# Kernel optimization log

Hardware: AMD Instinct MI355X
Metric: run time of the kernel (lower is better)

Reference implementation:

```python
import jax, jax.numpy as jnp
import numpy as np

VOCAB, EMB, HID, NTAG, SEQ = 50000, 256, 512, 20, 8192
H = HID // 2  # per-direction hidden size


def _lstm_dir(x, Wih, Whh, bih, bhh, reverse):
    # x: [S, E]; PyTorch gate order i, f, g, o
    h0 = jnp.zeros((H,), x.dtype)
    c0 = jnp.zeros((H,), x.dtype)
    b = bih + bhh
    xg = x @ Wih.T + b  # [S, 4H] precompute input projection

    def step(carry, xt):
        h, c = carry
        gates = xt + h @ Whh.T
        i, f, g, o = jnp.split(gates, 4)
        i = jax.nn.sigmoid(i)
        f = jax.nn.sigmoid(f)
        g = jnp.tanh(g)
        o = jax.nn.sigmoid(o)
        c = f * c + i * g
        h = o * jnp.tanh(c)
        return (h, c), h

    _, hs = jax.lax.scan(step, (h0, c0), xg, reverse=reverse)
    return hs  # [S, H]


def _viterbi(emissions, start_trans, end_trans, trans):
    # emissions [S, T]; torchcrf-style Viterbi decode
    score0 = start_trans + emissions[0]

    def fwd(score, em):
        tot = score[:, None] + trans          # [T_from, T_to]
        bp = jnp.argmax(tot, axis=0)          # best previous tag per next tag
        score = jnp.max(tot, axis=0) + em
        return score, bp

    final, bps = jax.lax.scan(fwd, score0, emissions[1:])
    final = final + end_trans
    last = jnp.argmax(final).astype(jnp.int32)

    def back(tag, bp):
        prev = bp[tag].astype(jnp.int32)
        return prev, prev

    _, prevs = jax.lax.scan(back, last, bps, reverse=True)
    return jnp.concatenate([prevs, last[None]])  # [S]


def setup_inputs() -> dict:
    key = jax.random.key(0)
    ks = jax.random.split(key, 16)
    s = 0.1
    inp = {
        "sentence": jax.random.randint(ks[0], (SEQ,), 0, VOCAB, dtype=jnp.int64)
                    if jax.config.read("jax_enable_x64") else
                    jax.random.randint(ks[0], (SEQ,), 0, VOCAB, dtype=jnp.int32),
        "embed": jax.random.normal(ks[1], (VOCAB, EMB), jnp.float32),
        "Wih_f": jax.random.normal(ks[2], (4 * H, EMB), jnp.float32) * s,
        "Whh_f": jax.random.normal(ks[3], (4 * H, H), jnp.float32) * s,
        "bih_f": jax.random.normal(ks[4], (4 * H,), jnp.float32) * s,
        "bhh_f": jax.random.normal(ks[5], (4 * H,), jnp.float32) * s,
        "Wih_b": jax.random.normal(ks[6], (4 * H, EMB), jnp.float32) * s,
        "Whh_b": jax.random.normal(ks[7], (4 * H, H), jnp.float32) * s,
        "bih_b": jax.random.normal(ks[8], (4 * H,), jnp.float32) * s,
        "bhh_b": jax.random.normal(ks[9], (4 * H,), jnp.float32) * s,
        "Wout": jax.random.normal(ks[10], (NTAG, HID), jnp.float32) * s,
        "bout": jax.random.normal(ks[11], (NTAG,), jnp.float32) * s,
        "start_trans": jax.random.normal(ks[12], (NTAG,), jnp.float32) * s,
        "end_trans": jax.random.normal(ks[13], (NTAG,), jnp.float32) * s,
        "trans": jax.random.normal(ks[14], (NTAG, NTAG), jnp.float32) * s,
    }
    return inp


def reference(sentence, embed, Wih_f, Whh_f, bih_f, bhh_f,
              Wih_b, Whh_b, bih_b, bhh_b, Wout, bout,
              start_trans, end_trans, trans):
    x = embed[sentence]                                  # [S, E]
    h_f = _lstm_dir(x, Wih_f, Whh_f, bih_f, bhh_f, reverse=False)
    h_b = _lstm_dir(x, Wih_b, Whh_b, bih_b, bhh_b, reverse=True)
    lstm_out = jnp.concatenate([h_f, h_b], axis=-1)      # [S, HID]; dropout is eval-mode identity
    emissions = lstm_out @ Wout.T + bout                 # [S, T]
    path = _viterbi(emissions, start_trans, end_trans, trans)
    return path
```

## Files before the change

### kernel.cpp

```cpp
#include <hip/hip_runtime.h>
#include <hip/hip_bf16.h>


#define S    8192
#define E    256
#define Hh   256
#define G    1024
#define NT   20
#define NB   4
#define NCHUNK 128
#define CLEN   64
#define SENT 0x7FC0DEADu

__global__ __launch_bounds__(256) void sentinel_fill(unsigned int* __restrict__ lo_u)
{
    size_t base = (size_t)blockIdx.x * 1024 + threadIdx.x;
    #pragma unroll
    for (int i = 0; i < 4; ++i)
        __hip_atomic_store(&lo_u[base + (size_t)i * 256], SENT,
                           __ATOMIC_RELAXED, __HIP_MEMORY_SCOPE_AGENT);
}

__global__ __launch_bounds__(1024, 4) void xg_project(
    const int* __restrict__ sent, const float* __restrict__ embed,
    const float* __restrict__ Wih_f, const float* __restrict__ bih_f, const float* __restrict__ bhh_f,
    const float* __restrict__ Wih_b, const float* __restrict__ bih_b, const float* __restrict__ bhh_b,
    float* __restrict__ xg)
{
    const int tb  = blockIdx.x;
    const int rb  = blockIdx.y;
    const int dir = blockIdx.z;
    const int tid = threadIdx.x;
    const int q   = tid >> 8;
    const int idx = tid & 255;
    const int r   = rb * 256 + idx;
    const float* Wih = dir ? Wih_b : Wih_f;

    __shared__ __align__(16) float4 xs4[32 * 64];
    __shared__ float psum[1024];

    const int t0 = tb * 32;
    #pragma unroll
    for (int i = 0; i < 2; ++i) {
        int qq  = i * 1024 + tid;
        int row = qq >> 6;
        int c4  = qq & 63;
        int widx = sent[t0 + row];
        xs4[qq] = *(const float4*)(embed + (size_t)widx * E + (size_t)c4 * 4);
    }

    float w[64];
    #pragma unroll
    for (int k = 0; k < 64; k += 4) {
        float4 v = *(const float4*)(Wih + (size_t)r * E + q * 64 + k);
        w[k] = v.x; w[k+1] = v.y; w[k+2] = v.z; w[k+3] = v.w;
    }
    float bias = 0.f;
    if (tid < 256) bias = dir ? (bih_b[r] + bhh_b[r]) : (bih_f[r] + bhh_f[r]);
    __syncthreads();

    const float* xs = (const float*)xs4 + q * 64;
    float* outb = xg + ((size_t)dir * S + t0) * G + r;
    for (int tt = 0; tt < 32; ++tt) {
        float a0 = 0.f, a1 = 0.f, a2 = 0.f, a3 = 0.f;
        #pragma unroll
        for (int k = 0; k < 64; k += 4) {
            float4 h4 = *(const float4*)(xs + tt * E + k);
            a0 = fmaf(w[k],   h4.x, a0);
            a1 = fmaf(w[k+1], h4.y, a1);
            a2 = fmaf(w[k+2], h4.z, a2);
            a3 = fmaf(w[k+3], h4.w, a3);
        }
        psum[tid] = (a0 + a1) + (a2 + a3);
        __syncthreads();
        if (tid < 256)
            outb[(size_t)tt * G] = bias +
                ((psum[idx] + psum[idx + 256]) + (psum[idx + 512] + psum[idx + 768]));
        __syncthreads();
    }
}

__global__ __launch_bounds__(1024, 4) void lstm_scan_mc(
    const float* __restrict__ xg,
    const float* __restrict__ Whh_f,
    const float* __restrict__ Whh_b,
    float* __restrict__ out)
{
    const int b    = blockIdx.x;
    const int dir  = blockIdx.y;
    const int tid  = threadIdx.x;
    const int q    = tid >> 8;
    const int idx  = tid & 255;
    const int gate = idx >> 6;
    const int hloc = idx & 63;
    const int hidx = b * 64 + hloc;
    const int row  = gate * Hh + hidx;
    const float* W   = dir ? Whh_b : Whh_f;
    const float* xgd = xg + (size_t)dir * S * G;

    float w[64];
    #pragma unroll
    for (int k = 0; k < 64; k += 4) {
        float4 v = *(const float4*)(W + (size_t)row * Hh + q * 64 + k);
        w[k] = v.x; w[k+1] = v.y; w[k+2] = v.z; w[k+3] = v.w;
    }

    __shared__ __align__(16) float h_lds[Hh];
    __shared__ float psum[1024];
    __shared__ float gates_lds[256];
    if (tid < Hh) h_lds[tid] = 0.f;
    float c = 0.f;

    const int t0 = dir ? (S - 1) : 0;
    const int dt = dir ? -1 : 1;
    float xg_cur = (tid < 256) ? xgd[(size_t)t0 * G + row] : 0.f;
    __syncthreads();

    for (int s = 0; s < S; ++s) {
        const int t = t0 + dt * s;
        float xg_next = 0.f;
        if (tid < 256 && s + 1 < S) xg_next = xgd[(size_t)(t + dt) * G + row];

        const float* hh = (const float*)h_lds + q * 64;
        float a0 = 0.f, a1 = 0.f, a2 = 0.f, a3 = 0.f;
        #pragma unroll
        for (int k = 0; k < 64; k += 4) {
            float4 h4 = *(const float4*)(hh + k);
            a0 = fmaf(w[k],   h4.x, a0);
            a1 = fmaf(w[k+1], h4.y, a1);
            a2 = fmaf(w[k+2], h4.z, a2);
            a3 = fmaf(w[k+3], h4.w, a3);
        }
        psum[tid] = (a0 + a1) + (a2 + a3);
        __syncthreads();

        if (tid < 256) {
            float acc = xg_cur +
                ((psum[idx] + psum[idx + 256]) + (psum[idx + 512] + psum[idx + 768]));
            float a = (gate == 2) ? tanhf(acc) : 1.f / (1.f + expf(-acc));
            gates_lds[idx] = a;
        }
        __syncthreads();

        if (tid < 64) {
            float iv = gates_lds[hloc];
            float fv = gates_lds[64 + hloc];
            float gv = gates_lds[128 + hloc];
            float ov = gates_lds[192 + hloc];
            c = fv * c + iv * gv;
            float h = ov * tanhf(c);
            __hip_atomic_store(out + (size_t)t * 512 + dir * Hh + hidx, h,
                               __ATOMIC_RELAXED, __HIP_MEMORY_SCOPE_AGENT);
            h_lds[hidx] = h;
        }
        if (s + 1 < S && tid < Hh && (tid >> 6) != b) {
            const unsigned int* srcp =
                (const unsigned int*)(out + (size_t)t * 512 + dir * Hh + tid);
            unsigned int v;
            do {
                v = __hip_atomic_load(srcp, __ATOMIC_RELAXED,
                                      __HIP_MEMORY_SCOPE_AGENT);
            } while (v == SENT);
            h_lds[tid] = __uint_as_float(v);
        }
        __syncthreads();
        xg_cur = xg_next;
    }
}

__global__ __launch_bounds__(256) void emissions_kernel(
    const float* __restrict__ lo,
    const float* __restrict__ Wout,
    const float* __restrict__ bout,
    float* __restrict__ em)
{
    int gid = blockIdx.x * blockDim.x + threadIdx.x;
    if (gid >= S * NT) return;
    int t = gid / NT;
    int j = gid - t * NT;
    const float* x = lo + (size_t)t * 512;
    const float* w = Wout + (size_t)j * 512;
    float a0 = 0.f, a1 = 0.f, a2 = 0.f, a3 = 0.f;
    #pragma unroll 8
    for (int k = 0; k < 512; k += 4) {
        float4 xv = *(const float4*)(x + k);
        float4 wv = *(const float4*)(w + k);
        a0 = fmaf(xv.x, wv.x, a0);
        a1 = fmaf(xv.y, wv.y, a1);
        a2 = fmaf(xv.z, wv.z, a2);
        a3 = fmaf(xv.w, wv.w, a3);
    }
    em[gid] = bout[j] + ((a0 + a1) + (a2 + a3));
}

__global__ __launch_bounds__(64) void viterbi_fwd(
    const float* __restrict__ em,
    const float* __restrict__ start_trans,
    const float* __restrict__ end_trans,
    const float* __restrict__ trans,
    unsigned char* __restrict__ bp,
    int* __restrict__ last_out)
{
    const int lane = threadIdx.x;
    const int g    = lane / 20;
    const int j    = lane - g * 20;
    const int i0   = g * 7;

    float tc[7];
    #pragma unroll
    for (int u = 0; u < 7; ++u) {
        int i = i0 + u;
        tc[u] = (g < 3 && i < 20) ? trans[i * NT + j] : -3.0e38f;
    }

    const int jj = (g < 3) ? j : 0;
    float snew  = start_trans[jj] + em[jj];
    if (g == 0) bp[j] = (unsigned char)j;
    float e_cur = em[NT + jj];

    for (int t = 1; t < S; ++t) {
        float s_sub[7];
        #pragma unroll
        for (int u = 0; u < 7; ++u)
            s_sub[u] = __shfl(snew, i0 + u);
        float e_nxt = (t + 1 < S) ? em[(size_t)(t + 1) * NT + jj] : 0.f;

        float bv = s_sub[0] + tc[0];
        int   bi = i0;
        #pragma unroll
        for (int u = 1; u < 7; ++u) {
            float v = s_sub[u] + tc[u];
            if (v > bv) { bv = v; bi = i0 + u; }
        }
        float v0 = __shfl(bv, jj), v1 = __shfl(bv, jj + 20), v2 = __shfl(bv, jj + 40);
        int   c0 = __shfl(bi, jj), c1 = __shfl(bi, jj + 20), c2 = __shfl(bi, jj + 40);
        float best = v0; int bidx = c0;
        if (v1 > best) { best = v1; bidx = c1; }
        if (v2 > best) { best = v2; bidx = c2; }
        snew = best + e_cur;
        if (g == 0) bp[(size_t)t * NT + j] = (unsigned char)bidx;
        e_cur = e_nxt;
    }

    float bv = __shfl(snew, 0) + end_trans[0];
    int   bi = 0;
    #pragma unroll 1
    for (int i = 1; i < 20; ++i) {
        float v = __shfl(snew, i) + end_trans[i];
        if (v > bv) { bv = v; bi = i; }
    }
    if (lane == 0) *last_out = bi;
}

__global__ __launch_bounds__(64) void bt_maps(
    const unsigned char* __restrict__ bp, unsigned char* __restrict__ maps)
{
    __shared__ unsigned char lbp[CLEN * NT];
    const int c = blockIdx.x, tid = threadIdx.x;
    const unsigned* src = (const unsigned*)(bp + (size_t)c * CLEN * NT);
    unsigned* dst = (unsigned*)lbp;
    for (int q = tid; q < CLEN * NT / 4; q += 64) dst[q] = src[q];
    __syncthreads();
    if (tid < NT) {
        int x = tid;
        for (int t = CLEN - 1; t >= 0; --t) x = lbp[t * NT + x];
        maps[c * NT + tid] = (unsigned char)x;
    }
}

__global__ __launch_bounds__(64) void bt_boundary(
    const unsigned char* __restrict__ maps, const int* __restrict__ last_out,
    int* __restrict__ btags)
{
    __shared__ unsigned char m[NCHUNK * NT];
    const int tid = threadIdx.x;
    for (int q = tid; q < NCHUNK * NT; q += 64) m[q] = maps[q];
    __syncthreads();
    if (tid == 0) {
        int x = *last_out;
        btags[NCHUNK - 1] = x;
        for (int c = NCHUNK - 1; c >= 1; --c) {
            x = m[c * NT + x];
            btags[c - 1] = x;
        }
    }
}

__global__ __launch_bounds__(64) void bt_emit(
    const unsigned char* __restrict__ bp, const int* __restrict__ btags,
    int* __restrict__ path)
{
    __shared__ unsigned char lbp[CLEN * NT];
    const int c = blockIdx.x, tid = threadIdx.x;
    const unsigned* src = (const unsigned*)(bp + (size_t)c * CLEN * NT);
    unsigned* dst = (unsigned*)lbp;
    for (int q = tid; q < CLEN * NT / 4; q += 64) dst[q] = src[q];
    __syncthreads();
    if (tid == 0) {
        int x = btags[c];
        path[c * CLEN + CLEN - 1] = x;
        for (int t = CLEN - 1; t >= 1; --t) {
            x = lbp[t * NT + x];
            path[c * CLEN + t - 1] = x;
        }
    }
}

extern "C" void kernel_launch(void* const* d_in, const int* in_sizes, int n_in,
                              void* d_out, int out_size, void* d_ws, size_t ws_size,
                              hipStream_t stream) {
    const int*   sent   = (const int*)  d_in[0];
    const float* embed  = (const float*)d_in[1];
    const float* Wih_f  = (const float*)d_in[2];
    const float* Whh_f  = (const float*)d_in[3];
    const float* bih_f  = (const float*)d_in[4];
    const float* bhh_f  = (const float*)d_in[5];
    const float* Wih_b  = (const float*)d_in[6];
    const float* Whh_b  = (const float*)d_in[7];
    const float* bih_b  = (const float*)d_in[8];
    const float* bhh_b  = (const float*)d_in[9];
    const float* Wout   = (const float*)d_in[10];
    const float* bout   = (const float*)d_in[11];
    const float* start_trans = (const float*)d_in[12];
    const float* end_trans   = (const float*)d_in[13];
    const float* trans       = (const float*)d_in[14];
    int* path = (int*)d_out;

    char* ws = (char*)d_ws;
    size_t off = 0;
    float* xg = (float*)(ws + off); off += (size_t)2 * S * G * 4;
    float* lo = (float*)(ws + off); off += (size_t)S * 512 * 4;
    float* em = (float*)(ws + off); off += (size_t)S * NT * 4;
    unsigned char* bp   = (unsigned char*)(ws + off); off += (size_t)S * NT;
    unsigned char* maps = (unsigned char*)(ws + off); off += 4096;
    int* btags = (int*)(ws + off); off += 1024;
    int* lastp = (int*)(ws + off); off += 256;

    sentinel_fill<<<dim3(4096), 256, 0, stream>>>((unsigned int*)lo);
    xg_project<<<dim3(S / 32, 4, 2), 1024, 0, stream>>>(
        sent, embed, Wih_f, bih_f, bhh_f, Wih_b, bih_b, bhh_b, xg);
    lstm_scan_mc<<<dim3(NB, 2), 1024, 0, stream>>>(xg, Whh_f, Whh_b, lo);
    emissions_kernel<<<dim3((S * NT + 255) / 256), 256, 0, stream>>>(lo, Wout, bout, em);
    viterbi_fwd<<<dim3(1), 64, 0, stream>>>(em, start_trans, end_trans, trans, bp, lastp);
    bt_maps<<<dim3(NCHUNK), 64, 0, stream>>>(bp, maps);
    bt_boundary<<<dim3(1), 64, 0, stream>>>(maps, lastp, btags);
    bt_emit<<<dim3(NCHUNK), 64, 0, stream>>>(bp, btags, path);
}
```

Measured before the change: 15.61 ms.

## Co-locate LSTM scan workgroups on one XCC and use cheaper cross-block polling

```diff
diff --git a/kernel.cpp b/kernel.cpp
--- a/kernel.cpp
+++ b/kernel.cpp
@@ -8,17 +8,42 @@
 #define G    1024
 #define NT   20
 #define NB   4
+#define NCAND 64
 #define NCHUNK 128
 #define CLEN   64
 #define SENT 0x7FC0DEADu
 
+struct ScanCtl {
+    int cnt[16];
+    int winner;
+};
+
+__device__ __forceinline__ int get_xcc_id() {
+    int x;
+    asm volatile("s_getreg_b32 %0, hwreg(HW_REG_XCC_ID)" : "=s"(x));
+    return x & 0xf;
+}
+
+__device__ __forceinline__ unsigned ld_sc0_u32(const void* p) {
+    unsigned v;
+    asm volatile("global_load_dword %0, %1, off sc0\n"
+                 "s_waitcnt vmcnt(0)"
+                 : "=v"(v) : "v"(p) : "memory");
+    return v;
+}
+
+__global__ __launch_bounds__(64) void init_ctl(ScanCtl* __restrict__ ctl)
+{
+    if (threadIdx.x < 16) ctl->cnt[threadIdx.x] = 0;
+    if (threadIdx.x == 0) ctl->winner = -1;
+}
+
 __global__ __launch_bounds__(256) void sentinel_fill(unsigned int* __restrict__ lo_u)
 {
     size_t base = (size_t)blockIdx.x * 1024 + threadIdx.x;
     #pragma unroll
     for (int i = 0; i < 4; ++i)
-        __hip_atomic_store(&lo_u[base + (size_t)i * 256], SENT,
-                           __ATOMIC_RELAXED, __HIP_MEMORY_SCOPE_AGENT);
+        lo_u[base + (size_t)i * 256] = SENT;
 }
 
 __global__ __launch_bounds__(1024, 4) void xg_project(
@@ -84,11 +109,29 @@
     const float* __restrict__ xg,
     const float* __restrict__ Whh_f,
     const float* __restrict__ Whh_b,
-    float* __restrict__ out)
-{
-    const int b    = blockIdx.x;
-    const int dir  = blockIdx.y;
-    const int tid  = threadIdx.x;
+    float* __restrict__ out,
+    ScanCtl* __restrict__ ctl)
+{
+    __shared__ int s_role;
+    const int tid = threadIdx.x;
+
+    if (tid == 0) {
+        int xcc = get_xcc_id();
+        int ticket = atomicAdd(&ctl->cnt[xcc], 1);
+        if (ticket == 7) atomicCAS(&ctl->winner, -1, xcc);
+        int wn;
+        do {
+            wn = __hip_atomic_load(&ctl->winner, __ATOMIC_RELAXED,
+                                   __HIP_MEMORY_SCOPE_AGENT);
+        } while (wn == -1);
+        s_role = (wn == xcc && ticket < 8) ? ticket : -1;
+    }
+    __syncthreads();
+    const int role = s_role;
+    if (role < 0) return;
+    const int b   = role & 3;
+    const int dir = role >> 2;
+
     const int q    = tid >> 8;
     const int idx  = tid & 255;
     const int gate = idx >> 6;
@@ -113,13 +156,17 @@
 
     const int t0 = dir ? (S - 1) : 0;
     const int dt = dir ? -1 : 1;
-    float xg_cur = (tid < 256) ? xgd[(size_t)t0 * G + row] : 0.f;
+    float xg_c = 0.f, xg_n1 = 0.f;
+    if (tid < 256) {
+        xg_c  = xgd[(size_t)t0 * G + row];
+        xg_n1 = xgd[(size_t)(t0 + dt) * G + row];
+    }
     __syncthreads();
 
     for (int s = 0; s < S; ++s) {
         const int t = t0 + dt * s;
-        float xg_next = 0.f;
-        if (tid < 256 && s + 1 < S) xg_next = xgd[(size_t)(t + dt) * G + row];
+        float xg_n2 = 0.f;
+        if (tid < 256 && s + 2 < S) xg_n2 = xgd[(size_t)(t + 2 * dt) * G + row];
 
         const float* hh = (const float*)h_lds + q * 64;
         float a0 = 0.f, a1 = 0.f, a2 = 0.f, a3 = 0.f;
@@ -135,7 +182,7 @@
         __syncthreads();
 
         if (tid < 256) {
-            float acc = xg_cur +
+            float acc = xg_c +
                 ((psum[idx] + psum[idx + 256]) + (psum[idx + 512] + psum[idx + 768]));
             float a = (gate == 2) ? tanhf(acc) : 1.f / (1.f + expf(-acc));
             gates_lds[idx] = a;
@@ -150,21 +197,26 @@
             c = fv * c + iv * gv;
             float h = ov * tanhf(c);
             __hip_atomic_store(out + (size_t)t * 512 + dir * Hh + hidx, h,
-                               __ATOMIC_RELAXED, __HIP_MEMORY_SCOPE_AGENT);
+                               __ATOMIC_RELAXED, __HIP_MEMORY_SCOPE_WORKGROUP);
             h_lds[hidx] = h;
         }
         if (s + 1 < S && tid < Hh && (tid >> 6) != b) {
             const unsigned int* srcp =
                 (const unsigned int*)(out + (size_t)t * 512 + dir * Hh + tid);
             unsigned int v;
+            int spins = 0;
             do {
-                v = __hip_atomic_load(srcp, __ATOMIC_RELAXED,
-                                      __HIP_MEMORY_SCOPE_AGENT);
+                if (++spins <= 64) {
+                    v = ld_sc0_u32(srcp);
+                } else {
+                    v = __hip_atomic_load(srcp, __ATOMIC_RELAXED,
+                                          __HIP_MEMORY_SCOPE_AGENT);
+                }
             } while (v == SENT);
             h_lds[tid] = __uint_as_float(v);
         }
         __syncthreads();
-        xg_cur = xg_next;
+        xg_c = xg_n1; xg_n1 = xg_n2;
     }
 }
 
@@ -335,11 +387,13 @@
     unsigned char* maps = (unsigned char*)(ws + off); off += 4096;
     int* btags = (int*)(ws + off); off += 1024;
     int* lastp = (int*)(ws + off); off += 256;
-
+    ScanCtl* ctl = (ScanCtl*)(ws + off); off += 256;
+
+    init_ctl<<<dim3(1), 64, 0, stream>>>(ctl);
     sentinel_fill<<<dim3(4096), 256, 0, stream>>>((unsigned int*)lo);
     xg_project<<<dim3(S / 32, 4, 2), 1024, 0, stream>>>(
         sent, embed, Wih_f, bih_f, bhh_f, Wih_b, bih_b, bhh_b, xg);
-    lstm_scan_mc<<<dim3(NB, 2), 1024, 0, stream>>>(xg, Whh_f, Whh_b, lo);
+    lstm_scan_mc<<<dim3(NCAND), 1024, 0, stream>>>(xg, Whh_f, Whh_b, lo, ctl);
     emissions_kernel<<<dim3((S * NT + 255) / 256), 256, 0, stream>>>(lo, Wout, bout, em);
     viterbi_fwd<<<dim3(1), 64, 0, stream>>>(em, start_trans, end_trans, trans, bp, lastp);
     bt_maps<<<dim3(NCHUNK), 64, 0, stream>>>(bp, maps);
```

Measured after the change: 54.63 ms. 3.5x slower.

## Split LSTM recurrence over K across blocks with tagged partial-sum exchange

Applied to the files above, without the earlier changes.

```diff
diff --git a/kernel.cpp b/kernel.cpp
--- a/kernel.cpp
+++ b/kernel.cpp
@@ -10,15 +10,11 @@
 #define NB   4
 #define NCHUNK 128
 #define CLEN   64
-#define SENT 0x7FC0DEADu
-
-__global__ __launch_bounds__(256) void sentinel_fill(unsigned int* __restrict__ lo_u)
-{
-    size_t base = (size_t)blockIdx.x * 1024 + threadIdx.x;
-    #pragma unroll
-    for (int i = 0; i < 4; ++i)
-        __hip_atomic_store(&lo_u[base + (size_t)i * 256], SENT,
-                           __ATOMIC_RELAXED, __HIP_MEMORY_SCOPE_AGENT);
+
+__global__ __launch_bounds__(1024) void pbuf_clear(unsigned long long* __restrict__ pbuf)
+{
+    int i = blockIdx.x * 1024 + threadIdx.x;
+    if (i < 2 * 2 * NB * 1024) pbuf[i] = 0ull;
 }
 
 __global__ __launch_bounds__(1024, 4) void xg_project(
@@ -80,91 +76,99 @@
     }
 }
 
-__global__ __launch_bounds__(1024, 4) void lstm_scan_mc(
+__global__ __launch_bounds__(1024, 4) void lstm_scan_k(
     const float* __restrict__ xg,
     const float* __restrict__ Whh_f,
     const float* __restrict__ Whh_b,
-    float* __restrict__ out)
+    float* __restrict__ out,
+    unsigned long long* __restrict__ pbuf)
 {
     const int b    = blockIdx.x;
     const int dir  = blockIdx.y;
     const int tid  = threadIdx.x;
-    const int q    = tid >> 8;
-    const int idx  = tid & 255;
-    const int gate = idx >> 6;
-    const int hloc = idx & 63;
-    const int hidx = b * 64 + hloc;
-    const int row  = gate * Hh + hidx;
     const float* W   = dir ? Whh_b : Whh_f;
     const float* xgd = xg + (size_t)dir * S * G;
 
     float w[64];
     #pragma unroll
     for (int k = 0; k < 64; k += 4) {
-        float4 v = *(const float4*)(W + (size_t)row * Hh + q * 64 + k);
+        float4 v = *(const float4*)(W + (size_t)tid * Hh + b * 64 + k);
         w[k] = v.x; w[k+1] = v.y; w[k+2] = v.z; w[k+3] = v.w;
     }
 
-    __shared__ __align__(16) float h_lds[Hh];
-    __shared__ float psum[1024];
-    __shared__ float gates_lds[256];
-    if (tid < Hh) h_lds[tid] = 0.f;
+    __shared__ __align__(16) float h_lds[64];
+    __shared__ float gl[256];
+    const bool cons = (((tid >> 6) & 3) == b);
+    const int  u    = tid & 63;
+    const int  gate = tid >> 8;
+    if (tid < 64) h_lds[tid] = 0.f;
     float c = 0.f;
 
     const int t0 = dir ? (S - 1) : 0;
     const int dt = dir ? -1 : 1;
-    float xg_cur = (tid < 256) ? xgd[(size_t)t0 * G + row] : 0.f;
+    float xg_c = 0.f, xg_n1 = 0.f;
+    if (cons) {
+        xg_c  = xgd[(size_t)t0 * G + tid];
+        xg_n1 = xgd[(size_t)(t0 + dt) * G + tid];
+    }
+    const int p0 = (b + 1) & 3, p1 = (b + 2) & 3, p2 = (b + 3) & 3;
     __syncthreads();
 
     for (int s = 0; s < S; ++s) {
         const int t = t0 + dt * s;
-        float xg_next = 0.f;
-        if (tid < 256 && s + 1 < S) xg_next = xgd[(size_t)(t + dt) * G + row];
-
-        const float* hh = (const float*)h_lds + q * 64;
+        float xg_n2 = 0.f;
+        if (cons && s + 2 < S) xg_n2 = xgd[(size_t)(t + 2 * dt) * G + tid];
+
         float a0 = 0.f, a1 = 0.f, a2 = 0.f, a3 = 0.f;
         #pragma unroll
         for (int k = 0; k < 64; k += 4) {
-            float4 h4 = *(const float4*)(hh + k);
+            float4 h4 = *(const float4*)(h_lds + k);
             a0 = fmaf(w[k],   h4.x, a0);
             a1 = fmaf(w[k+1], h4.y, a1);
             a2 = fmaf(w[k+2], h4.z, a2);
             a3 = fmaf(w[k+3], h4.w, a3);
         }
-        psum[tid] = (a0 + a1) + (a2 + a3);
+        const float part = (a0 + a1) + (a2 + a3);
+
+        const unsigned st = (unsigned)(s + 1);
+        const size_t base = (size_t)((dir * 2) + (s & 1)) * (NB * 1024);
+        unsigned long long pw =
+            ((unsigned long long)st << 32) | (unsigned long long)__float_as_uint(part);
+        __hip_atomic_store(&pbuf[base + (size_t)b * 1024 + tid], pw,
+                           __ATOMIC_RELAXED, __HIP_MEMORY_SCOPE_AGENT);
+
+        if (cons) {
+            const unsigned long long* q0 = &pbuf[base + (size_t)p0 * 1024 + tid];
+            const unsigned long long* q1 = &pbuf[base + (size_t)p1 * 1024 + tid];
+            const unsigned long long* q2 = &pbuf[base + (size_t)p2 * 1024 + tid];
+            unsigned long long u0, u1, u2;
+            do {
+                u0 = __hip_atomic_load(q0, __ATOMIC_RELAXED, __HIP_MEMORY_SCOPE_AGENT);
+                u1 = __hip_atomic_load(q1, __ATOMIC_RELAXED, __HIP_MEMORY_SCOPE_AGENT);
+                u2 = __hip_atomic_load(q2, __ATOMIC_RELAXED, __HIP_MEMORY_SCOPE_AGENT);
+            } while ((unsigned)(u0 >> 32) != st || (unsigned)(u1 >> 32) != st ||
+                     (unsigned)(u2 >> 32) != st);
+            float acc = xg_c + part;
+            acc += __uint_as_float((unsigned)u0);
+            acc += __uint_as_float((unsigned)u1);
+            acc += __uint_as_float((unsigned)u2);
+            float a = (gate == 2) ? tanhf(acc) : 1.f / (1.f + expf(-acc));
+            gl[gate * 64 + u] = a;
+        }
         __syncthreads();
 
-        if (tid < 256) {
-            float acc = xg_cur +
-                ((psum[idx] + psum[idx + 256]) + (psum[idx + 512] + psum[idx + 768]));
-            float a = (gate == 2) ? tanhf(acc) : 1.f / (1.f + expf(-acc));
-            gates_lds[idx] = a;
-        }
-        __syncthreads();
-
         if (tid < 64) {
-            float iv = gates_lds[hloc];
-            float fv = gates_lds[64 + hloc];
-            float gv = gates_lds[128 + hloc];
-            float ov = gates_lds[192 + hloc];
+            float iv = gl[tid];
+            float fv = gl[64 + tid];
+            float gv = gl[128 + tid];
+            float ov = gl[192 + tid];
             c = fv * c + iv * gv;
             float h = ov * tanhf(c);
-            __hip_atomic_store(out + (size_t)t * 512 + dir * Hh + hidx, h,
-                               __ATOMIC_RELAXED, __HIP_MEMORY_SCOPE_AGENT);
-            h_lds[hidx] = h;
-        }
-        if (s + 1 < S && tid < Hh && (tid >> 6) != b) {
-            const unsigned int* srcp =
-                (const unsigned int*)(out + (size_t)t * 512 + dir * Hh + tid);
-            unsigned int v;
-            do {
-                v = __hip_atomic_load(srcp, __ATOMIC_RELAXED,
-                                      __HIP_MEMORY_SCOPE_AGENT);
-            } while (v == SENT);
-            h_lds[tid] = __uint_as_float(v);
+            h_lds[tid] = h;
+            out[(size_t)t * 512 + dir * Hh + b * 64 + tid] = h;
         }
         __syncthreads();
-        xg_cur = xg_next;
+        xg_c = xg_n1; xg_n1 = xg_n2;
     }
 }
 
@@ -335,11 +339,13 @@
     unsigned char* maps = (unsigned char*)(ws + off); off += 4096;
     int* btags = (int*)(ws + off); off += 1024;
     int* lastp = (int*)(ws + off); off += 256;
-
-    sentinel_fill<<<dim3(4096), 256, 0, stream>>>((unsigned int*)lo);
+    off = (off + 255) & ~(size_t)255;
+    unsigned long long* pbuf = (unsigned long long*)(ws + off); off += 2 * 2 * NB * 1024 * 8;
+
+    pbuf_clear<<<dim3(16), 1024, 0, stream>>>(pbuf);
     xg_project<<<dim3(S / 32, 4, 2), 1024, 0, stream>>>(
         sent, embed, Wih_f, bih_f, bhh_f, Wih_b, bih_b, bhh_b, xg);
-    lstm_scan_mc<<<dim3(NB, 2), 1024, 0, stream>>>(xg, Whh_f, Whh_b, lo);
+    lstm_scan_k<<<dim3(NB, 2), 1024, 0, stream>>>(xg, Whh_f, Whh_b, lo, pbuf);
     emissions_kernel<<<dim3((S * NT + 255) / 256), 256, 0, stream>>>(lo, Wout, bout, em);
     viterbi_fwd<<<dim3(1), 64, 0, stream>>>(em, start_trans, end_trans, trans, bp, lastp);
     bt_maps<<<dim3(NCHUNK), 64, 0, stream>>>(bp, maps);
```

Result: slower. 18.10 ms (+15.9%).

## Replace sentinel polling with step-tagged double-buffered handoff and co-located blocks

Applied to the files above, without the earlier changes.

```diff
diff --git a/kernel.cpp b/kernel.cpp
--- a/kernel.cpp
+++ b/kernel.cpp
@@ -10,15 +10,27 @@
 #define NB   4
 #define NCHUNK 128
 #define CLEN   64
-#define SENT 0x7FC0DEADu
-
-__global__ __launch_bounds__(256) void sentinel_fill(unsigned int* __restrict__ lo_u)
-{
-    size_t base = (size_t)blockIdx.x * 1024 + threadIdx.x;
-    #pragma unroll
-    for (int i = 0; i < 4; ++i)
-        __hip_atomic_store(&lo_u[base + (size_t)i * 256], SENT,
-                           __ATOMIC_RELAXED, __HIP_MEMORY_SCOPE_AGENT);
+#define MAGICV 0xC0FFEE00DEADBEEFull
+
+#define SB_SLOW 1024
+#define SB_HSH  2048
+#define SB_HSS  2056
+#define SB_CTR  2064
+#define SB_SIZE 2080
+
+__device__ __forceinline__ unsigned long long ld_sc0_u64(const unsigned long long* p) {
+    unsigned long long v;
+    asm volatile("global_load_dwordx2 %0, %1, off sc0\n\ts_waitcnt vmcnt(0)"
+                 : "=v"(v) : "v"(p) : "memory");
+    return v;
+}
+
+__global__ __launch_bounds__(1024) void sync_init(unsigned long long* __restrict__ sb)
+{
+    int i = threadIdx.x;
+    sb[i] = 0ull;
+    sb[1024 + i] = 0ull;
+    if (i < SB_SIZE - 2048) sb[2048 + i] = 0ull;
 }
 
 __global__ __launch_bounds__(1024, 4) void xg_project(
@@ -80,15 +92,52 @@
     }
 }
 
-__global__ __launch_bounds__(1024, 4) void lstm_scan_mc(
+__global__ __launch_bounds__(1024, 4) void lstm_scan_hs(
     const float* __restrict__ xg,
     const float* __restrict__ Whh_f,
     const float* __restrict__ Whh_b,
-    float* __restrict__ out)
-{
-    const int b    = blockIdx.x;
-    const int dir  = blockIdx.y;
-    const int tid  = threadIdx.x;
+    float* __restrict__ out,
+    unsigned long long* __restrict__ sb)
+{
+    const int bid = blockIdx.x;
+    if (bid & 7) return;
+    const int role = bid >> 3;
+    const int b   = role & 3;
+    const int dir = role >> 2;
+    const int tid = threadIdx.x;
+
+    unsigned long long* hot     = sb;
+    unsigned long long* slow    = sb + SB_SLOW;
+    unsigned long long* hs_hot  = sb + SB_HSH;
+    unsigned long long* hs_slow = sb + SB_HSS;
+    int* ctr = (int*)(sb + SB_CTR);
+
+    __shared__ int s_fast;
+    if (tid == 0) s_fast = 1;
+    __syncthreads();
+    if (tid == 0) {
+        __hip_atomic_store(&hs_hot[role], MAGICV,
+                           __ATOMIC_RELAXED, __HIP_MEMORY_SCOPE_WORKGROUP);
+        __hip_atomic_store(&hs_slow[role], MAGICV,
+                           __ATOMIC_RELAXED, __HIP_MEMORY_SCOPE_AGENT);
+    }
+    if (tid < 8 && tid != role) {
+        bool seen = false;
+        for (int it = 0; it < 1024 && !seen; ++it)
+            seen = (ld_sc0_u64(&hs_hot[tid]) == MAGICV);
+        if (!seen) s_fast = 0;
+        while (__hip_atomic_load(&hs_slow[tid], __ATOMIC_RELAXED,
+                                 __HIP_MEMORY_SCOPE_AGENT) != MAGICV) {}
+    }
+    __syncthreads();
+    int use_fast = s_fast;
+    if (tid == 0) {
+        __hip_atomic_fetch_add(ctr, 1, __ATOMIC_RELAXED, __HIP_MEMORY_SCOPE_AGENT);
+        while (__hip_atomic_load(ctr, __ATOMIC_RELAXED,
+                                 __HIP_MEMORY_SCOPE_AGENT) < 8) {}
+    }
+    __syncthreads();
+
     const int q    = tid >> 8;
     const int idx  = tid & 255;
     const int gate = idx >> 6;
@@ -113,13 +162,18 @@
 
     const int t0 = dir ? (S - 1) : 0;
     const int dt = dir ? -1 : 1;
-    float xg_cur = (tid < 256) ? xgd[(size_t)t0 * G + row] : 0.f;
+    float xg_c = 0.f, xg_n1 = 0.f;
+    if (tid < 256) {
+        xg_c  = xgd[(size_t)t0 * G + row];
+        xg_n1 = xgd[(size_t)(t0 + dt) * G + row];
+    }
+    const bool poller = (tid < Hh) && ((tid >> 6) != b);
     __syncthreads();
 
     for (int s = 0; s < S; ++s) {
         const int t = t0 + dt * s;
-        float xg_next = 0.f;
-        if (tid < 256 && s + 1 < S) xg_next = xgd[(size_t)(t + dt) * G + row];
+        float xg_n2 = 0.f;
+        if (tid < 256 && s + 2 < S) xg_n2 = xgd[(size_t)(t + 2 * dt) * G + row];
 
         const float* hh = (const float*)h_lds + q * 64;
         float a0 = 0.f, a1 = 0.f, a2 = 0.f, a3 = 0.f;
@@ -135,12 +189,15 @@
         __syncthreads();
 
         if (tid < 256) {
-            float acc = xg_cur +
+            float acc = xg_c +
                 ((psum[idx] + psum[idx + 256]) + (psum[idx + 512] + psum[idx + 768]));
             float a = (gate == 2) ? tanhf(acc) : 1.f / (1.f + expf(-acc));
             gates_lds[idx] = a;
         }
         __syncthreads();
+
+        const int slot = ((dir << 1) | (s & 1)) << 8;
+        const unsigned st = (unsigned)(s + 1);
 
         if (tid < 64) {
             float iv = gates_lds[hloc];
@@ -149,22 +206,35 @@
             float ov = gates_lds[192 + hloc];
             c = fv * c + iv * gv;
             float h = ov * tanhf(c);
-            __hip_atomic_store(out + (size_t)t * 512 + dir * Hh + hidx, h,
+            unsigned long long pw =
+                ((unsigned long long)st << 32) | (unsigned long long)__float_as_uint(h);
+            __hip_atomic_store(&hot[slot + hidx], pw,
+                               __ATOMIC_RELAXED, __HIP_MEMORY_SCOPE_WORKGROUP);
+            __hip_atomic_store(&slow[slot + hidx], pw,
                                __ATOMIC_RELAXED, __HIP_MEMORY_SCOPE_AGENT);
+            out[(size_t)t * 512 + dir * Hh + hidx] = h;
             h_lds[hidx] = h;
         }
-        if (s + 1 < S && tid < Hh && (tid >> 6) != b) {
-            const unsigned int* srcp =
-                (const unsigned int*)(out + (size_t)t * 512 + dir * Hh + tid);
-            unsigned int v;
-            do {
-                v = __hip_atomic_load(srcp, __ATOMIC_RELAXED,
-                                      __HIP_MEMORY_SCOPE_AGENT);
-            } while (v == SENT);
-            h_lds[tid] = __uint_as_float(v);
+        if (s + 1 < S && poller) {
+            unsigned long long v = 0; bool got = false;
+            if (use_fast) {
+                #pragma unroll 1
+                for (int spins = 0; spins < 4096; ++spins) {
+                    v = ld_sc0_u64(&hot[slot + tid]);
+                    if ((unsigned)(v >> 32) == st) { got = true; break; }
+                }
+                if (!got) use_fast = 0;
+            }
+            if (!got) {
+                do {
+                    v = __hip_atomic_load(&slow[slot + tid], __ATOMIC_RELAXED,
+                                          __HIP_MEMORY_SCOPE_AGENT);
+                } while ((unsigned)(v >> 32) != st);
+            }
+            h_lds[tid] = __uint_as_float((unsigned)v);
         }
         __syncthreads();
-        xg_cur = xg_next;
+        xg_c = xg_n1; xg_n1 = xg_n2;
     }
 }
 
@@ -335,11 +405,13 @@
     unsigned char* maps = (unsigned char*)(ws + off); off += 4096;
     int* btags = (int*)(ws + off); off += 1024;
     int* lastp = (int*)(ws + off); off += 256;
-
-    sentinel_fill<<<dim3(4096), 256, 0, stream>>>((unsigned int*)lo);
+    off = (off + 255) & ~(size_t)255;
+    unsigned long long* sb = (unsigned long long*)(ws + off); off += SB_SIZE * 8;
+
+    sync_init<<<dim3(1), 1024, 0, stream>>>(sb);
     xg_project<<<dim3(S / 32, 4, 2), 1024, 0, stream>>>(
         sent, embed, Wih_f, bih_f, bhh_f, Wih_b, bih_b, bhh_b, xg);
-    lstm_scan_mc<<<dim3(NB, 2), 1024, 0, stream>>>(xg, Whh_f, Whh_b, lo);
+    lstm_scan_hs<<<dim3(64), 1024, 0, stream>>>(xg, Whh_f, Whh_b, lo, sb);
     emissions_kernel<<<dim3((S * NT + 255) / 256), 256, 0, stream>>>(lo, Wout, bout, em);
     viterbi_fwd<<<dim3(1), 64, 0, stream>>>(em, start_trans, end_trans, trans, bp, lastp);
     bt_maps<<<dim3(NCHUNK), 64, 0, stream>>>(bp, maps);
```

After: 17.16 ms. 9.9% more time.
